# Kernel optimization log

Measured on AMD Instinct MI355X. Metric: run time of the kernel, lower is better.

Reference implementation:

```python
import jax, jax.numpy as jnp
import numpy as np

N_HEAD = 16
N_KV = 4
HEAD_DIM = 128
N_EMBD = 2048
GATE_CH = 32


def setup_inputs() -> dict:
    key = jax.random.key(0)
    ks = jax.random.split(key, 9)
    B, T = 2, 2048
    return {
        "x": jax.random.normal(ks[0], (B, T, N_EMBD), jnp.float32),
        "ve": jax.random.normal(ks[1], (B, T, N_KV * HEAD_DIM), jnp.float32),
        "cos": jax.random.uniform(ks[2], (T, 1, HEAD_DIM // 2), jnp.float32),
        "sin": jax.random.uniform(ks[3], (T, 1, HEAD_DIM // 2), jnp.float32),
        "wq": jax.random.normal(ks[4], (N_HEAD * HEAD_DIM, N_EMBD), jnp.float32) * 0.02,
        "wk": jax.random.normal(ks[5], (N_KV * HEAD_DIM, N_EMBD), jnp.float32) * 0.02,
        "wv": jax.random.normal(ks[6], (N_KV * HEAD_DIM, N_EMBD), jnp.float32) * 0.02,
        "wo": jax.random.normal(ks[7], (N_EMBD, N_EMBD), jnp.float32) * 0.02,
        "wgate": jax.random.normal(ks[8], (N_KV, GATE_CH), jnp.float32) * 0.02,
        "window_size": 512,
    }


def _rope(t, cos, sin):
    half = t.shape[-1] // 2
    t1, t2 = t[..., :half], t[..., half:]
    return jnp.concatenate([t1 * cos + t2 * sin, -t1 * sin + t2 * cos], axis=-1)


def _rms(t):
    eps = jnp.finfo(t.dtype).eps
    return t * jax.lax.rsqrt(jnp.mean(t * t, axis=-1, keepdims=True) + eps)


def reference(x, ve, cos, sin, wq, wk, wv, wo, wgate, window_size):
    B, T, _ = x.shape
    q = (x @ wq.T).reshape(B, T, N_HEAD, HEAD_DIM)
    k = (x @ wk.T).reshape(B, T, N_KV, HEAD_DIM)
    v = (x @ wv.T).reshape(B, T, N_KV, HEAD_DIM)
    # value-embedding gate
    gate = 2.0 * jax.nn.sigmoid(x[..., :GATE_CH] @ wgate.T)  # [B,T,N_KV]
    v = v + gate[..., None] * ve.reshape(B, T, N_KV, HEAD_DIM)
    # RoPE then QK RMSNorm
    q = _rms(_rope(q, cos, sin)).transpose(0, 2, 1, 3)  # [B,H,T,D]
    k = _rms(_rope(k, cos, sin)).transpose(0, 2, 1, 3)  # [B,KV,T,D]
    v = v.transpose(0, 2, 1, 3)
    rep = N_HEAD // N_KV
    k = jnp.repeat(k, rep, axis=1)  # repeat_interleave over head dim
    v = jnp.repeat(v, rep, axis=1)
    # sliding-window causal mask (past_len=0, key_len=T)
    pos = jnp.arange(T)
    mask = (pos[None, :] <= pos[:, None]) & (pos[None, :] >= pos[:, None] - window_size + 1)
    scale = 1.0 / jnp.sqrt(jnp.float32(HEAD_DIM))
    scores = jnp.einsum("bhqd,bhkd->bhqk", q, k) * scale
    scores = jnp.where(mask[None, None], scores, jnp.finfo(scores.dtype).min)
    attn = jax.nn.softmax(scores, axis=-1)
    y = jnp.einsum("bhqk,bhkd->bhqd", attn, v)
    y = y.transpose(0, 2, 1, 3).reshape(B, T, N_EMBD)
    return y @ wo.T
```

## Files before the change

kernel.cpp:

```cpp
#include <hip/hip_runtime.h>
#include <hip/hip_bf16.h>

typedef __attribute__((ext_vector_type(8))) short short8_t;
typedef __attribute__((ext_vector_type(4))) float f32x4;
typedef __attribute__((ext_vector_type(16))) float f32x16;
using bf16 = __hip_bfloat16;

#define MFMA_BF16(A, B, C) __builtin_amdgcn_mfma_f32_16x16x32_bf16((A), (B), (C), 0, 0, 0)
#define MFMA32_BF16(A, B, C) __builtin_amdgcn_mfma_f32_32x32x16_bf16((A), (B), (C), 0, 0, 0)

#define GLD_LDS16(g, l)                                                        \
  __builtin_amdgcn_global_load_lds(                                           \
      (const __attribute__((address_space(1))) unsigned int*)(const void*)(g),\
      (__attribute__((address_space(3))) unsigned int*)(void*)(l), 16, 0, 0)

__device__ __forceinline__ float bits2f(short s) {
  union { unsigned int u; float f; } c;
  c.u = ((unsigned int)(unsigned short)s) << 16;
  return c.f;
}
__device__ __forceinline__ short f2bits(float f) {
  bf16 h = __float2bfloat16(f);
  return *reinterpret_cast<short*>(&h);
}
__device__ __forceinline__ unsigned pack2(float lo, float hi) {
  return ((unsigned)(unsigned short)f2bits(lo)) |
         (((unsigned)(unsigned short)f2bits(hi)) << 16);
}
__device__ __forceinline__ float exp2_(float x) {
#if __has_builtin(__builtin_amdgcn_exp2f)
  return __builtin_amdgcn_exp2f(x);
#else
  return exp2f(x);
#endif
}

__global__ __launch_bounds__(256) void cvt_all(const float* __restrict__ x,
                                               const float* __restrict__ wq,
                                               const float* __restrict__ wk,
                                               const float* __restrict__ wv,
                                               const float* __restrict__ wo,
                                               short* __restrict__ xb,
                                               short* __restrict__ wqkvb,
                                               short* __restrict__ wob) {
  int i = (blockIdx.x * 256 + threadIdx.x) * 4;
  const float* src;
  short* dst;
  if (i < 8388608) {
    src = x + i; dst = xb + i;
  } else if (i < 14680064) {
    int j = i - 8388608;
    dst = wqkvb + j;
    if (j < 4194304) src = wq + j;
    else if (j < 5242880) src = wk + (j - 4194304);
    else src = wv + (j - 5242880);
  } else {
    int j = i - 14680064;
    src = wo + j; dst = wob + j;
  }
  float4 v = *reinterpret_cast<const float4*>(src);
  short4 o;
  o.x = f2bits(v.x); o.y = f2bits(v.y); o.z = f2bits(v.z); o.w = f2bits(v.w);
  *reinterpret_cast<short4*>(dst) = o;
}

template <int STORE_BF16, int FUSED>
__global__ __launch_bounds__(256, 2) void gemm_bt4(
    const short* __restrict__ A, const short* __restrict__ Bt,
    void* __restrict__ C, int M, int N, int K, int CM, int CN,
    short* __restrict__ qO, short* __restrict__ kO, short* __restrict__ vTO,
    const float* __restrict__ cosT, const float* __restrict__ sinT,
    const float* __restrict__ x32, const float* __restrict__ ve32,
    const float* __restrict__ wg32) {
  __shared__ __align__(16) char smem[FUSED ? 67584 : 65536];
  short* lds = (short*)smem;
  const int c = (int)blockIdx.x & 7;
  const int i = (int)blockIdx.x >> 3;
  const int cmi = c & 3, cni = c >> 2;
  const int m0 = (cmi * CM + (i % CM)) * 128;
  const int n0 = (cni * CN + (i / CM)) * 128;

  const int tid = threadIdx.x, w = tid >> 6, lane = tid & 63;
  const int wr = w >> 1, wc = w & 1;
  const int rr = lane & 15, g = lane >> 4;

  const int srow = tid >> 3;
  const int gc = (tid & 7) ^ (srow & 7);
  const short* Asrc = A + (size_t)(m0 + srow) * K + gc * 8;
  const short* Bsrc = Bt + (size_t)(n0 + srow) * K + gc * 8;
  const size_t rstep = (size_t)32 * K;
  const int dofs = tid * 16;

  const int abase = (((wr * 64 + rr) << 7) | (g << 4)) ^ ((rr & 7) << 4);
  const int bbase = ((((wc * 64 + rr) << 7) | (g << 4)) ^ ((rr & 7) << 4)) + 16384;

  f32x4 acc[4][4];
#pragma unroll
  for (int mi = 0; mi < 4; ++mi)
#pragma unroll
    for (int ni = 0; ni < 4; ++ni) acc[mi][ni] = (f32x4){0.f, 0.f, 0.f, 0.f};

  const int nt = K >> 6;

#define STAGE4(t, bufbyte) do {                                                \
    const short* a_ = Asrc + (size_t)(t) * 64;                                 \
    const short* b_ = Bsrc + (size_t)(t) * 64;                                 \
    char* la_ = (char*)lds + (bufbyte) + dofs;                                 \
    GLD_LDS16(a_,             la_);                                            \
    GLD_LDS16(a_ + rstep,     la_ + 4096);                                     \
    GLD_LDS16(a_ + 2 * rstep, la_ + 8192);                                     \
    GLD_LDS16(a_ + 3 * rstep, la_ + 12288);                                    \
    GLD_LDS16(b_,             la_ + 16384);                                    \
    GLD_LDS16(b_ + rstep,     la_ + 20480);                                    \
    GLD_LDS16(b_ + 2 * rstep, la_ + 24576);                                    \
    GLD_LDS16(b_ + 3 * rstep, la_ + 28672);                                    \
  } while (0)

  STAGE4(0, 0);
  asm volatile("s_waitcnt vmcnt(0)" ::: "memory");
  asm volatile("s_barrier" ::: "memory");

  int cur = 0;
  for (int t = 0; t < nt; ++t) {
    if (t + 1 < nt) STAGE4(t + 1, cur ^ 32768);
    const char* bufp = (const char*)lds + cur;
#pragma unroll
    for (int kk = 0; kk < 2; ++kk) {
      const int ko = kk * 64;
      short8_t a0 = *(const short8_t*)(bufp + ((abase ^ ko)));
      short8_t a1 = *(const short8_t*)(bufp + ((abase ^ ko) + 2048));
      short8_t a2 = *(const short8_t*)(bufp + ((abase ^ ko) + 4096));
      short8_t a3 = *(const short8_t*)(bufp + ((abase ^ ko) + 6144));
      short8_t b0 = *(const short8_t*)(bufp + ((bbase ^ ko)));
      short8_t b1 = *(const short8_t*)(bufp + ((bbase ^ ko) + 2048));
      short8_t b2 = *(const short8_t*)(bufp + ((bbase ^ ko) + 4096));
      short8_t b3 = *(const short8_t*)(bufp + ((bbase ^ ko) + 6144));
      __builtin_amdgcn_s_setprio(1);
      acc[0][0] = MFMA_BF16(a0, b0, acc[0][0]);
      acc[0][1] = MFMA_BF16(a0, b1, acc[0][1]);
      acc[0][2] = MFMA_BF16(a0, b2, acc[0][2]);
      acc[0][3] = MFMA_BF16(a0, b3, acc[0][3]);
      acc[1][0] = MFMA_BF16(a1, b0, acc[1][0]);
      acc[1][1] = MFMA_BF16(a1, b1, acc[1][1]);
      acc[1][2] = MFMA_BF16(a1, b2, acc[1][2]);
      acc[1][3] = MFMA_BF16(a1, b3, acc[1][3]);
      acc[2][0] = MFMA_BF16(a2, b0, acc[2][0]);
      acc[2][1] = MFMA_BF16(a2, b1, acc[2][1]);
      acc[2][2] = MFMA_BF16(a2, b2, acc[2][2]);
      acc[2][3] = MFMA_BF16(a2, b3, acc[2][3]);
      acc[3][0] = MFMA_BF16(a3, b0, acc[3][0]);
      acc[3][1] = MFMA_BF16(a3, b1, acc[3][1]);
      acc[3][2] = MFMA_BF16(a3, b2, acc[3][2]);
      acc[3][3] = MFMA_BF16(a3, b3, acc[3][3]);
      __builtin_amdgcn_s_setprio(0);
    }
    if (t + 1 < nt) {
      asm volatile("s_waitcnt vmcnt(0)" ::: "memory");
      asm volatile("s_barrier" ::: "memory");
    }
    cur ^= 32768;
  }
#undef STAGE4

  if (!FUSED) {
#pragma unroll
    for (int mi = 0; mi < 4; ++mi)
#pragma unroll
      for (int ni = 0; ni < 4; ++ni) {
        const int row = m0 + wr * 64 + mi * 16 + g * 4;
        const int col = n0 + wc * 64 + ni * 16 + rr;
#pragma unroll
        for (int j = 0; j < 4; ++j) {
          float v = acc[mi][ni][j];
          if (STORE_BF16)
            reinterpret_cast<short*>(C)[(size_t)(row + j) * N + col] = f2bits(v);
          else
            reinterpret_cast<float*>(C)[(size_t)(row + j) * N + col] = v;
        }
      }
    return;
  }

  __syncthreads();
  const int slot = n0 >> 7;

  if (slot < 20) {
    float* S = (float*)smem;
#pragma unroll
    for (int mi = 0; mi < 4; ++mi)
#pragma unroll
      for (int ni = 0; ni < 4; ++ni) {
        int r0 = wr * 64 + mi * 16 + g * 4;
        int cl = wc * 64 + ni * 16 + rr;
#pragma unroll
        for (int j = 0; j < 4; ++j) S[(r0 + j) * 132 + cl] = acc[mi][ni][j];
      }
    __syncthreads();
    int row = tid >> 1, u = tid & 1;
    int mglob = m0 + row;
    int bb = mglob >> 11, tk = mglob & 2047;
    const float* Sr = S + row * 132 + u * 32;
    const float* cp = cosT + tk * 64 + u * 32;
    const float* sp = sinT + tk * 64 + u * 32;
    float o1[32], o2[32];
    float ss = 0.f;
#pragma unroll
    for (int ii = 0; ii < 32; ++ii) {
      float t1 = Sr[ii], t2 = Sr[ii + 64];
      float cv = cp[ii], sv = sp[ii];
      o1[ii] = t1 * cv + t2 * sv;
      o2[ii] = t2 * cv - t1 * sv;
      ss += o1[ii] * o1[ii] + o2[ii] * o2[ii];
    }
    ss += __shfl_xor(ss, 1, 64);
    float r = rsqrtf(ss * (1.f / 128.f) + 1.1920929e-07f);
    short* dst;
    if (slot < 16) {
      r *= 0.08838834764831845f * 1.4426950408889634f;
      dst = qO + ((size_t)(bb * 16 + slot) * 2048 + tk) * 128 + u * 32;
    } else {
      dst = kO + ((size_t)(bb * 4 + (slot - 16)) * 2048 + tk) * 128 + u * 32;
    }
#pragma unroll
    for (int v8 = 0; v8 < 4; ++v8) {
      short8_t s1, s2;
#pragma unroll
      for (int k2 = 0; k2 < 8; ++k2) {
        s1[k2] = f2bits(o1[v8 * 8 + k2] * r);
        s2[k2] = f2bits(o2[v8 * 8 + k2] * r);
      }
      *(short8_t*)(dst + v8 * 8) = s1;
      *(short8_t*)(dst + 64 + v8 * 8) = s2;
    }
  } else {
    const int kv = slot - 20;
    short* TL = (short*)smem;
    float* GL = (float*)(smem + 32768);
    {
      int row = tid >> 1, u = tid & 1;
      size_t mglob = (size_t)(m0 + row);
      const float* xp = x32 + mglob * 2048 + u * 16;
      const float* wg = wg32 + kv * 32 + u * 16;
      float z = 0.f;
#pragma unroll
      for (int ii = 0; ii < 16; ++ii) z += xp[ii] * wg[ii];
      z += __shfl_xor(z, 1, 64);
      if (!u) GL[row] = 2.f / (1.f + __expf(-z));
    }
    __syncthreads();
#pragma unroll
    for (int mi = 0; mi < 4; ++mi)
#pragma unroll
      for (int ni = 0; ni < 4; ++ni) {
        int r0 = wr * 64 + mi * 16 + g * 4;
        int cl = wc * 64 + ni * 16 + rr;
#pragma unroll
        for (int j = 0; j < 4; ++j) {
          int rw = r0 + j;
          float gate = GL[rw];
          float ev = ve32[(size_t)(m0 + rw) * 512 + kv * 128 + cl];
          float v = acc[mi][ni][j] + gate * ev;
          int byte = ((cl << 8) + (rw << 1)) ^ ((cl & 7) << 4);
          *(short*)((char*)TL + byte) = f2bits(v);
        }
      }
    __syncthreads();
    int d = tid >> 1, th = tid & 1;
    int bb = m0 >> 11, t0l = m0 & 2047;
    short* vdst = vTO + ((size_t)(bb * 4 + kv) * 128 + d) * 2048 + t0l + th * 64;
    const char* TLp = (const char*)TL;
#pragma unroll
    for (int g2 = 0; g2 < 8; ++g2) {
      short8_t o = *(const short8_t*)(TLp + (((d << 8) + th * 128 + g2 * 16) ^ ((d & 7) << 4)));
      *(short8_t*)(vdst + g2 * 8) = o;
    }
  }
}

__global__ __launch_bounds__(512) void attn_sw4(const short* __restrict__ Q,
                                                const short* __restrict__ K,
                                                const short* __restrict__ VT,
                                                short* __restrict__ Y,
                                                const int* __restrict__ winp) {
  const int T = 2048, H = 16;
  const int win = *winp;
  int combo = blockIdx.x & 7;
  int j = blockIdx.x >> 3;
  int b = combo >> 2, kvh = combo & 3;
  int q0 = (31 - j) * 64;

  __shared__ __align__(16) short Ks[2][64 * 128];
  __shared__ __align__(16) short Vs[2][128 * 64];

  int tid = threadIdx.x, w = tid >> 6, lane = tid & 63;
  int ql = lane & 31, hi = lane >> 5;
  int h = kvh * 4 + (w >> 1);
  int qrow = q0 + (w & 1) * 32 + ql;

  const short* qbase = Q + ((size_t)(b * H + h) * T + qrow) * 128;
  short8_t qf[8];
#pragma unroll
  for (int ks = 0; ks < 8; ++ks)
    qf[ks] = *reinterpret_cast<const short8_t*>(qbase + ks * 16 + hi * 8);

  const short* kbase = K + (size_t)(b * 4 + kvh) * T * 128;
  const short* vtbase = VT + (size_t)(b * 4 + kvh) * 128 * T;

  f32x16 acc[4];
#pragma unroll
  for (int dt = 0; dt < 4; ++dt)
#pragma unroll
    for (int r = 0; r < 16; ++r) acc[dt][r] = 0.f;
  float mreg = -1e30f, lsum = 0.f;

  int lo = q0 - win + 1;
  if (lo < 0) lo = 0;
  lo &= ~63;
  const int nt = (q0 + 64 - lo) >> 6;
  int qmin = q0 + (w & 1) * 32, qmax = qmin + 31;

#define STAGE_A(ti, bi) do {                                                   \
    int kc_ = lo + (ti) * 64;                                                  \
    _Pragma("unroll")                                                          \
    for (int r = 0; r < 2; ++r) {                                              \
      int seg = r * 8 + w;                                                     \
      int slot = seg * 64 + lane;                                              \
      int krow = slot >> 4;                                                    \
      int gc = (slot & 15) ^ (krow & 7);                                       \
      GLD_LDS16(kbase + (size_t)(kc_ + krow) * 128 + gc * 8,                   \
                (char*)Ks[bi] + seg * 1024);                                   \
    }                                                                          \
    _Pragma("unroll")                                                          \
    for (int r = 0; r < 2; ++r) {                                              \
      int seg = r * 8 + w;                                                     \
      int slot = seg * 64 + lane;                                              \
      int d_ = slot >> 3;                                                      \
      int gc = (slot & 7) ^ (d_ & 7);                                          \
      GLD_LDS16(vtbase + (size_t)d_ * T + kc_ + gc * 8,                        \
                (char*)Vs[bi] + seg * 1024);                                   \
    }                                                                          \
  } while (0)

  STAGE_A(0, 0);

  int cur = 0;
  for (int t = 0; t < nt; ++t) {
    if (t + 1 < nt) {
      STAGE_A(t + 1, cur ^ 1);
      asm volatile("s_waitcnt vmcnt(4)" ::: "memory");
    } else {
      asm volatile("s_waitcnt vmcnt(0)" ::: "memory");
    }
    asm volatile("s_barrier" ::: "memory");

    int kc = lo + t * 64;
    bool active = (kc <= qmax) && (kc + 63 >= qmin - win + 1);
    if (active) {
      const char* Kp = (const char*)Ks[cur];
      const char* Vp = (const char*)Vs[cur];
      f32x16 sA[2];
#pragma unroll
      for (int r = 0; r < 16; ++r) { sA[0][r] = 0.f; sA[1][r] = 0.f; }
#pragma unroll
      for (int kt = 0; kt < 2; ++kt) {
        int kr = kt * 32 + ql;
#pragma unroll
        for (int ks = 0; ks < 8; ++ks) {
          int byte = kr * 256 + (((ks * 2 + hi) ^ (kr & 7)) << 4);
          short8_t kf = *reinterpret_cast<const short8_t*>(Kp + byte);
          sA[kt] = MFMA32_BF16(kf, qf[ks], sA[kt]);
        }
      }
      float pmax = -1e30f;
#pragma unroll
      for (int kt = 0; kt < 2; ++kt)
#pragma unroll
        for (int r = 0; r < 16; ++r) {
          int key = kc + kt * 32 + (r & 3) + 8 * (r >> 2) + 4 * hi;
          float sv = sA[kt][r];
          sv = ((unsigned)(qrow - key) < (unsigned)win) ? sv : -1e30f;
          sA[kt][r] = sv;
          pmax = fmaxf(pmax, sv);
        }
      pmax = fmaxf(pmax, __shfl_xor(pmax, 32, 64));
      float mn = fmaxf(mreg, pmax);
      float corr = exp2_(mreg - mn);
      mreg = mn;
      float rs = 0.f;
#pragma unroll
      for (int kt = 0; kt < 2; ++kt)
#pragma unroll
        for (int r = 0; r < 16; ++r) {
          float p = exp2_(sA[kt][r] - mn);
          sA[kt][r] = p;
          rs += p;
        }
      rs += __shfl_xor(rs, 32, 64);
      lsum = lsum * corr + rs;
#pragma unroll
      for (int dt = 0; dt < 4; ++dt)
#pragma unroll
        for (int r = 0; r < 16; ++r) acc[dt][r] *= corr;

#pragma unroll
      for (int kt = 0; kt < 2; ++kt)
#pragma unroll
        for (int s = 0; s < 2; ++s) {
          unsigned a = pack2(sA[kt][8 * s + 0], sA[kt][8 * s + 1]);
          unsigned bb = pack2(sA[kt][8 * s + 2], sA[kt][8 * s + 3]);
          unsigned c = pack2(sA[kt][8 * s + 4], sA[kt][8 * s + 5]);
          unsigned dd = pack2(sA[kt][8 * s + 6], sA[kt][8 * s + 7]);
          unsigned sa = __shfl_xor(a, 32, 64);
          unsigned sb = __shfl_xor(bb, 32, 64);
          unsigned sc2 = __shfl_xor(c, 32, 64);
          unsigned sd = __shfl_xor(dd, 32, 64);
          union { unsigned u[4]; short8_t s8; } pu;
          pu.u[0] = hi ? sc2 : a;
          pu.u[1] = hi ? sd : bb;
          pu.u[2] = hi ? c : sa;
          pu.u[3] = hi ? dd : sb;
          const int kst = kt * 2 + s;
#pragma unroll
          for (int dt = 0; dt < 4; ++dt) {
            int d_ = dt * 32 + ql;
            int byte = (d_ << 7) + ((((kst * 2 + hi)) ^ (d_ & 7)) << 4);
            short8_t vf = *reinterpret_cast<const short8_t*>(Vp + byte);
            acc[dt] = MFMA32_BF16(vf, pu.s8, acc[dt]);
          }
        }
    }
    asm volatile("s_barrier" ::: "memory");
    cur ^= 1;
  }
#undef STAGE_A

  float rinv = 1.f / lsum;
  short* ybase = Y + ((size_t)(b * T + qrow) * H + h) * 128;
#pragma unroll
  for (int dt = 0; dt < 4; ++dt)
#pragma unroll
    for (int g2 = 0; g2 < 4; ++g2) {
      short4 o;
      o.x = f2bits(acc[dt][g2 * 4 + 0] * rinv);
      o.y = f2bits(acc[dt][g2 * 4 + 1] * rinv);
      o.z = f2bits(acc[dt][g2 * 4 + 2] * rinv);
      o.w = f2bits(acc[dt][g2 * 4 + 3] * rinv);
      *reinterpret_cast<short4*>(ybase + dt * 32 + 8 * g2 + 4 * hi) = o;
    }
}

extern "C" void kernel_launch(void* const* d_in, const int* in_sizes, int n_in,
                              void* d_out, int out_size, void* d_ws, size_t ws_size,
                              hipStream_t stream) {
  const float* x = (const float*)d_in[0];
  const float* ve = (const float*)d_in[1];
  const float* cosT = (const float*)d_in[2];
  const float* sinT = (const float*)d_in[3];
  const float* wq = (const float*)d_in[4];
  const float* wk = (const float*)d_in[5];
  const float* wv = (const float*)d_in[6];
  const float* wo = (const float*)d_in[7];
  const float* wgate = (const float*)d_in[8];
  const int* winp = (const int*)d_in[9];
  float* out = (float*)d_out;
  char* ws = (char*)d_ws;

  short* xb    = (short*)(ws);
  short* wqkvb = (short*)(ws + 16777216);
  short* wob   = (short*)(ws + 29360128);
  short* qpost = (short*)(ws + 62914560);
  short* kpost = (short*)(ws + 79691776);
  short* vTb   = (short*)(ws + 83886080);
  short* ybuf  = (short*)(ws + 88080384);

  cvt_all<<<dim3(18432), 256, 0, stream>>>(x, wq, wk, wv, wo, xb, wqkvb, wob);

  gemm_bt4<1, 1><<<dim3(768), 256, 0, stream>>>(
      xb, wqkvb, nullptr, 4096, 3072, 2048, 8, 12,
      qpost, kpost, vTb, cosT, sinT, x, ve, wgate);

  attn_sw4<<<dim3(256), 512, 0, stream>>>(qpost, kpost, vTb, ybuf, winp);

  gemm_bt4<0, 0><<<dim3(512), 256, 0, stream>>>(
      ybuf, wob, out, 4096, 2048, 2048, 8, 8,
      nullptr, nullptr, nullptr, nullptr, nullptr, nullptr, nullptr, nullptr);
}
```

Before: 159.6 us.

## Remap B columns so RoPE pairs stay in registers, drop LDS staging

New measurement: 159.1 us (median of 2 runs). Within noise of the previous version (-0.3%).

```diff
diff --git a/kernel.cpp b/kernel.cpp
--- a/kernel.cpp
+++ b/kernel.cpp
@@ -72,7 +72,7 @@
     const float* __restrict__ cosT, const float* __restrict__ sinT,
     const float* __restrict__ x32, const float* __restrict__ ve32,
     const float* __restrict__ wg32) {
-  __shared__ __align__(16) char smem[FUSED ? 67584 : 65536];
+  __shared__ __align__(16) char smem[65536];
   short* lds = (short*)smem;
   const int c = (int)blockIdx.x & 7;
   const int i = (int)blockIdx.x >> 3;
@@ -92,7 +92,11 @@
   const int dofs = tid * 16;
 
   const int abase = (((wr * 64 + rr) << 7) | (g << 4)) ^ ((rr & 7) << 4);
-  const int bbase = ((((wc * 64 + rr) << 7) | (g << 4)) ^ ((rr & 7) << 4)) + 16384;
+  const int brow = (FUSED ? wc * 32 : wc * 64) + rr;
+  const int bbase = (((brow << 7) | (g << 4)) ^ ((rr & 7) << 4)) + 16384;
+  const int BO1 = 2048;
+  const int BO2 = FUSED ? 8192 : 4096;
+  const int BO3 = FUSED ? 10240 : 6144;
 
   f32x4 acc[4][4];
 #pragma unroll
@@ -132,9 +136,9 @@
       short8_t a2 = *(const short8_t*)(bufp + ((abase ^ ko) + 4096));
       short8_t a3 = *(const short8_t*)(bufp + ((abase ^ ko) + 6144));
       short8_t b0 = *(const short8_t*)(bufp + ((bbase ^ ko)));
-      short8_t b1 = *(const short8_t*)(bufp + ((bbase ^ ko) + 2048));
-      short8_t b2 = *(const short8_t*)(bufp + ((bbase ^ ko) + 4096));
-      short8_t b3 = *(const short8_t*)(bufp + ((bbase ^ ko) + 6144));
+      short8_t b1 = *(const short8_t*)(bufp + ((bbase ^ ko) + BO1));
+      short8_t b2 = *(const short8_t*)(bufp + ((bbase ^ ko) + BO2));
+      short8_t b3 = *(const short8_t*)(bufp + ((bbase ^ ko) + BO3));
       __builtin_amdgcn_s_setprio(1);
       acc[0][0] = MFMA_BF16(a0, b0, acc[0][0]);
       acc[0][1] = MFMA_BF16(a0, b1, acc[0][1]);
@@ -185,53 +189,73 @@
   const int slot = n0 >> 7;
 
   if (slot < 20) {
-    float* S = (float*)smem;
+    const bool isq = slot < 16;
+    const int colL = wc * 32 + rr;
+    float o1v[4][2][4], o2v[4][2][4], ssp[4][4];
 #pragma unroll
     for (int mi = 0; mi < 4; ++mi)
 #pragma unroll
-      for (int ni = 0; ni < 4; ++ni) {
-        int r0 = wr * 64 + mi * 16 + g * 4;
-        int cl = wc * 64 + ni * 16 + rr;
-#pragma unroll
-        for (int j = 0; j < 4; ++j) S[(r0 + j) * 132 + cl] = acc[mi][ni][j];
+      for (int j = 0; j < 4; ++j) {
+        int rw = wr * 64 + mi * 16 + g * 4 + j;
+        int tk = (m0 + rw) & 2047;
+        float ss = 0.f;
+#pragma unroll
+        for (int ni = 0; ni < 2; ++ni) {
+          int cl = colL + ni * 16;
+          float cv = cosT[tk * 64 + cl];
+          float sv = sinT[tk * 64 + cl];
+          float lo = acc[mi][ni][j], hi = acc[mi][ni + 2][j];
+          float a = lo * cv + hi * sv;
+          float b2 = hi * cv - lo * sv;
+          o1v[mi][ni][j] = a;
+          o2v[mi][ni][j] = b2;
+          ss += a * a + b2 * b2;
+        }
+        ssp[mi][j] = ss;
       }
+#pragma unroll
+    for (int mi = 0; mi < 4; ++mi)
+#pragma unroll
+      for (int j = 0; j < 4; ++j) {
+#pragma unroll
+        for (int off = 1; off < 16; off <<= 1)
+          ssp[mi][j] += __shfl_xor(ssp[mi][j], off, 64);
+      }
+    float* P = (float*)smem;
+    if (rr == 0) {
+#pragma unroll
+      for (int mi = 0; mi < 4; ++mi)
+#pragma unroll
+        for (int j = 0; j < 4; ++j) {
+          int rw = wr * 64 + mi * 16 + g * 4 + j;
+          P[rw * 2 + wc] = ssp[mi][j];
+        }
+    }
     __syncthreads();
-    int row = tid >> 1, u = tid & 1;
-    int mglob = m0 + row;
-    int bb = mglob >> 11, tk = mglob & 2047;
-    const float* Sr = S + row * 132 + u * 32;
-    const float* cp = cosT + tk * 64 + u * 32;
-    const float* sp = sinT + tk * 64 + u * 32;
-    float o1[32], o2[32];
-    float ss = 0.f;
-#pragma unroll
-    for (int ii = 0; ii < 32; ++ii) {
-      float t1 = Sr[ii], t2 = Sr[ii + 64];
-      float cv = cp[ii], sv = sp[ii];
-      o1[ii] = t1 * cv + t2 * sv;
-      o2[ii] = t2 * cv - t1 * sv;
-      ss += o1[ii] * o1[ii] + o2[ii] * o2[ii];
-    }
-    ss += __shfl_xor(ss, 1, 64);
-    float r = rsqrtf(ss * (1.f / 128.f) + 1.1920929e-07f);
-    short* dst;
-    if (slot < 16) {
-      r *= 0.08838834764831845f * 1.4426950408889634f;
-      dst = qO + ((size_t)(bb * 16 + slot) * 2048 + tk) * 128 + u * 32;
-    } else {
-      dst = kO + ((size_t)(bb * 4 + (slot - 16)) * 2048 + tk) * 128 + u * 32;
-    }
-#pragma unroll
-    for (int v8 = 0; v8 < 4; ++v8) {
-      short8_t s1, s2;
-#pragma unroll
-      for (int k2 = 0; k2 < 8; ++k2) {
-        s1[k2] = f2bits(o1[v8 * 8 + k2] * r);
-        s2[k2] = f2bits(o2[v8 * 8 + k2] * r);
+    const float qs = 0.08838834764831845f * 1.4426950408889634f;
+#pragma unroll
+    for (int mi = 0; mi < 4; ++mi)
+#pragma unroll
+      for (int j = 0; j < 4; ++j) {
+        int rw = wr * 64 + mi * 16 + g * 4 + j;
+        int mglob = m0 + rw;
+        int bb = mglob >> 11, tk = mglob & 2047;
+        float sst = P[rw * 2] + P[rw * 2 + 1];
+        float r = rsqrtf(sst * (1.f / 128.f) + 1.1920929e-07f);
+        short* dst;
+        if (isq) {
+          r *= qs;
+          dst = qO + ((size_t)(bb * 16 + slot) * 2048 + tk) * 128;
+        } else {
+          dst = kO + ((size_t)(bb * 4 + (slot - 16)) * 2048 + tk) * 128;
+        }
+#pragma unroll
+        for (int ni = 0; ni < 2; ++ni) {
+          int cl = colL + ni * 16;
+          dst[cl] = f2bits(o1v[mi][ni][j] * r);
+          dst[cl + 64] = f2bits(o2v[mi][ni][j] * r);
+        }
       }
-      *(short8_t*)(dst + v8 * 8) = s1;
-      *(short8_t*)(dst + 64 + v8 * 8) = s2;
-    }
   } else {
     const int kv = slot - 20;
     short* TL = (short*)smem;
@@ -253,7 +277,7 @@
 #pragma unroll
       for (int ni = 0; ni < 4; ++ni) {
         int r0 = wr * 64 + mi * 16 + g * 4;
-        int cl = wc * 64 + ni * 16 + rr;
+        int cl = (ni >> 1) * 64 + wc * 32 + (ni & 1) * 16 + rr;
 #pragma unroll
         for (int j = 0; j < 4; ++j) {
           int rw = r0 + j;
```
